# Performance work log

Hardware: AMD Instinct MI355X
Metric: run time of the kernel (lower is better)

The kernel has to match this reference:

```python
import jax, jax.numpy as jnp
import numpy as np

B, C, H, W = 4, 96, 64, 64
CS = 8                      # chunk size
DN = 2 * C                  # d_inner (expand=2)
N = 16                      # d_state
K = 4                       # scan directions
DT_R = (C + 15) // 16       # dt_rank = ceil(d_model/16)
EPS = 1e-5


def _ln(x, g, b):
    m = x.mean(-1, keepdims=True)
    v = ((x - m) ** 2).mean(-1, keepdims=True)
    return (x - m) / jnp.sqrt(v + EPS) * g + b


def _selective_scan(xs, delta, A, Bs, Cs, D):
    # xs, delta: (Bc, K, Dn, L); Bs, Cs: (Bc, K, N, L); A: (K, Dn, N); D: (K, Dn)
    Bc, Kk, Dn, L = xs.shape
    uT = xs.transpose(3, 0, 1, 2)       # (L, Bc, K, Dn)
    dT = delta.transpose(3, 0, 1, 2)
    BT = Bs.transpose(3, 0, 1, 2)       # (L, Bc, K, N)
    CT = Cs.transpose(3, 0, 1, 2)

    def step(h, inp):
        u_l, d_l, B_l, C_l = inp
        dA = jnp.exp(d_l[..., None] * A)                       # (Bc,K,Dn,N)
        h = h * dA + (d_l * u_l)[..., None] * B_l[:, :, None, :]
        y = jnp.einsum('bkdn,bkn->bkd', h, C_l)
        return h, y

    h0 = jnp.zeros((Bc, Kk, Dn, A.shape[-1]), xs.dtype)
    _, ys = jax.lax.scan(step, h0, (uT, dT, BT, CT))           # ys: (L,Bc,K,Dn)
    ys = ys.transpose(1, 2, 3, 0)                              # (Bc,K,Dn,L)
    return ys + D[None, :, :, None] * xs


def _ss2d(xh, in_proj_w, conv_w, conv_b, x_proj_w, dt_w, dt_b,
          A_logs, Ds, outnorm_g, outnorm_b, out_proj_w):
    # xh: (Bc, Hc, Wc, C)
    Bc, Hc, Wc, _ = xh.shape
    L = Hc * Wc
    xz = xh @ in_proj_w                                        # (Bc,Hc,Wc,2*Dn)
    xc, z = jnp.split(xz, 2, axis=-1)
    xc = xc.transpose(0, 3, 1, 2)                              # (Bc,Dn,Hc,Wc)
    xc = jax.lax.conv_general_dilated(xc, conv_w, (1, 1), ((1, 1), (1, 1)),
                                      feature_group_count=DN)
    xc = jax.nn.silu(xc + conv_b[None, :, None, None])
    x0 = xc.reshape(Bc, DN, L)                                 # HW order
    x1 = xc.transpose(0, 1, 3, 2).reshape(Bc, DN, L)           # WH order
    xs = jnp.stack([x0, x1, x0[:, :, ::-1], x1[:, :, ::-1]], axis=1)  # (Bc,4,Dn,L)
    x_dbl = jnp.einsum('bkdl,kcd->bkcl', xs, x_proj_w)         # (Bc,4,DT_R+2N,L)
    dts = x_dbl[:, :, :DT_R]
    Bs = x_dbl[:, :, DT_R:DT_R + N]
    Cs = x_dbl[:, :, DT_R + N:]
    dts = jnp.einsum('bkrl,kdr->bkdl', dts, dt_w)
    delta = jax.nn.softplus(dts + dt_b[None, :, :, None])      # (Bc,4,Dn,L)
    A = -jnp.exp(A_logs).reshape(K, DN, N)
    ys = _selective_scan(xs, delta, A, Bs, Cs, Ds.reshape(K, DN))
    y0 = ys[:, 0]
    y1 = ys[:, 1].reshape(Bc, DN, Wc, Hc).transpose(0, 1, 3, 2).reshape(Bc, DN, L)
    y2 = ys[:, 2, :, ::-1]
    y3 = ys[:, 3, :, ::-1].reshape(Bc, DN, Wc, Hc).transpose(0, 1, 3, 2).reshape(Bc, DN, L)
    y = (y0 + y1 + y2 + y3).transpose(0, 2, 1)                 # (Bc,L,Dn)
    y = _ln(y, outnorm_g, outnorm_b).reshape(Bc, Hc, Wc, DN)
    y = y * jax.nn.silu(z)
    return y @ out_proj_w                                      # (Bc,Hc,Wc,C)


def reference(x, gamma, beta, alpha, ln1_g, ln1_b, in_proj_w, conv_w, conv_b,
              x_proj_w, dt_w, dt_b, A_logs, Ds, outnorm_g, outnorm_b, out_proj_w):
    Bb, Cc, Hh, Ww = x.shape
    # StateNorm: per (b, c) over spatial dims, unbiased=False
    mean = x.mean(axis=(2, 3), keepdims=True)
    var = ((x - mean) ** 2).mean(axis=(2, 3), keepdims=True)
    x_norm = (x - mean) / jnp.sqrt(var + EPS)
    x_norm = gamma[None, :, None, None] * x_norm + beta[None, :, None, None]
    x_act = jax.nn.silu(x_norm)                 # act_quant with bits=32 is identity
    hn, wn = Hh // CS, Ww // CS
    # chunk: b c (hn cs)(wn cs) -> (b hn wn) c cs cs
    xc = x_act.reshape(Bb, Cc, hn, CS, wn, CS).transpose(0, 2, 4, 1, 3, 5)
    xc = xc.reshape(Bb * hn * wn, Cc, CS, CS)
    # VSSBlock: h + SS2D(LN(h)) in BHWC (drop_path = identity at inference)
    h = xc.transpose(0, 2, 3, 1)                # (Bc, cs, cs, C)
    h = h + _ss2d(_ln(h, ln1_g, ln1_b), in_proj_w, conv_w, conv_b, x_proj_w,
                  dt_w, dt_b, A_logs, Ds, outnorm_g, outnorm_b, out_proj_w)
    xv = h.transpose(0, 3, 1, 2)                # back to BCHW
    # unchunk
    xv = xv.reshape(Bb, hn, wn, Cc, CS, CS).transpose(0, 3, 1, 4, 2, 5)
    xv = xv.reshape(Bb, Cc, Hh, Ww)
    return x + alpha * xv


def setup_inputs() -> dict:
    key = jax.random.key(0)
    ks = jax.random.split(key, 12)
    s = 0.02
    inp = {
        'x': jax.random.normal(ks[0], (B, C, H, W), jnp.float32),
        'gamma': jnp.ones((C,), jnp.float32),
        'beta': jnp.zeros((C,), jnp.float32),
        'alpha': jnp.float32(0.5),
        'ln1_g': jnp.ones((C,), jnp.float32),
        'ln1_b': jnp.zeros((C,), jnp.float32),
        'in_proj_w': jax.random.normal(ks[1], (C, 2 * DN), jnp.float32) / np.sqrt(C),
        'conv_w': jax.random.normal(ks[2], (DN, 1, 3, 3), jnp.float32) / 3.0,
        'conv_b': jnp.zeros((DN,), jnp.float32),
        'x_proj_w': jax.random.normal(ks[3], (K, DT_R + 2 * N, DN), jnp.float32) / np.sqrt(DN),
        'dt_w': jax.random.normal(ks[4], (K, DN, DT_R), jnp.float32) * (DT_R ** -0.5),
        'dt_b': jnp.full((K, DN), -4.6, jnp.float32) + s * jax.random.normal(ks[5], (K, DN), jnp.float32),
        'A_logs': jnp.log(jnp.broadcast_to(jnp.arange(1, N + 1, dtype=jnp.float32), (K * DN, N))).copy(),
        'Ds': jnp.ones((K * DN,), jnp.float32),
        'outnorm_g': jnp.ones((DN,), jnp.float32),
        'outnorm_b': jnp.zeros((DN,), jnp.float32),
        'out_proj_w': jax.random.normal(ks[6], (DN, C), jnp.float32) / np.sqrt(DN),
    }
    return inp
```

## Files before the change

kernel.cpp:

```cpp
#include <hip/hip_runtime.h>
#include <math.h>

__device__ __forceinline__ float siluf_(float x) {
    return x / (1.f + __expf(-x));
}

__device__ __forceinline__ int sperm(int k, int l) {
    int t = (k & 1) ? (((l & 7) << 3) | (l >> 3)) : l;
    return (k & 2) ? (63 - t) : t;
}

__device__ __forceinline__ unsigned int f2bf(float f) {
    unsigned int u = __float_as_uint(f);
    return (u + 0x7FFFu + ((u >> 16) & 1u)) >> 16;
}
__device__ __forceinline__ float bf2f(unsigned int h) {
    return __uint_as_float(h << 16);
}
__device__ __forceinline__ unsigned int packbf(float lo, float hi) {
    return f2bf(lo) | (f2bf(hi) << 16);
}

__global__ void k1a_stats(const float* __restrict__ x, float* __restrict__ stats) {
    int bc = blockIdx.x;
    const float* xp = x + (size_t)bc * 4096;
    float s = 0.f, sq = 0.f;
    for (int i = threadIdx.x; i < 4096; i += 256) {
        float v = xp[i]; s += v; sq += v * v;
    }
    __shared__ float rs[256], rq[256];
    rs[threadIdx.x] = s; rq[threadIdx.x] = sq;
    __syncthreads();
    for (int off = 128; off > 0; off >>= 1) {
        if (threadIdx.x < off) {
            rs[threadIdx.x] += rs[threadIdx.x + off];
            rq[threadIdx.x] += rq[threadIdx.x + off];
        }
        __syncthreads();
    }
    if (threadIdx.x == 0) {
        float m = rs[0] * (1.f / 4096.f);
        float v = rq[0] * (1.f / 4096.f) - m * m;
        stats[bc] = m;
        stats[384 + bc] = rsqrtf(v + 1e-5f);
    }
}

__global__ __launch_bounds__(256) void kAB(
        const float* __restrict__ x, const float* __restrict__ stats,
        const float* __restrict__ gamma, const float* __restrict__ beta,
        const float* __restrict__ ln1_g, const float* __restrict__ ln1_b,
        const float* __restrict__ Win,
        const float* __restrict__ conv_w, const float* __restrict__ conv_b,
        float* __restrict__ x0T_all,
        unsigned int* __restrict__ zg_b) {
    int blk = blockIdx.x;
    int xcd = blk & 7, j = blk >> 3;
    int chunk = xcd * 32 + (j >> 1), cg = j & 1;
    int b = chunk >> 6, chh = (chunk >> 3) & 7, chw = chunk & 7;
    __shared__ float hs[64 * 97];
    __shared__ float xc[96 * 65];
    int t = threadIdx.x;
    for (int i = t; i < 6144; i += 256) {
        int c = i >> 6, pos = i & 63;
        int bc = b * 96 + c;
        int hh = chh * 8 + (pos >> 3), ww = chw * 8 + (pos & 7);
        float v = x[(((size_t)bc) * 64 + hh) * 64 + ww];
        float xn = (v - stats[bc]) * stats[384 + bc] * gamma[c] + beta[c];
        hs[pos * 97 + c] = siluf_(xn);
    }
    __syncthreads();
    {
        int p = t >> 2, o = t & 3;
        float s = 0.f, sq = 0.f;
        #pragma unroll
        for (int jj = 0; jj < 24; jj++) { float v = hs[p * 97 + o + 4 * jj]; s += v; sq += v * v; }
        s += __shfl_xor(s, 1); sq += __shfl_xor(sq, 1);
        s += __shfl_xor(s, 2); sq += __shfl_xor(sq, 2);
        float m = s * (1.f / 96.f);
        float rinv = rsqrtf(sq * (1.f / 96.f) - m * m + 1e-5f);
        #pragma unroll
        for (int jj = 0; jj < 24; jj++) {
            int c = o + 4 * jj;
            hs[p * 97 + c] = (hs[p * 97 + c] - m) * rinv * ln1_g[c] + ln1_b[c];
        }
    }
    __syncthreads();
    {
        int p = t & 63;
        int wv = __builtin_amdgcn_readfirstlane(t >> 6);
        int jc = cg * 96 + wv * 24;
        int jz = 192 + jc;
        float acc[48];
        #pragma unroll
        for (int i = 0; i < 48; i++) acc[i] = 0.f;
        for (int c = 0; c < 96; c++) {
            float u = hs[p * 97 + c];
            const float* w = Win + c * 384;
            #pragma unroll
            for (int i = 0; i < 24; i++) acc[i] = fmaf(u, w[jc + i], acc[i]);
            #pragma unroll
            for (int i = 0; i < 24; i++) acc[24 + i] = fmaf(u, w[jz + i], acc[24 + i]);
        }
        #pragma unroll
        for (int i = 0; i < 24; i++) xc[(wv * 24 + i) * 65 + p] = acc[i];
        int i2base = cg * 48 + wv * 12;
        unsigned int* o_ = zg_b + (size_t)chunk * 6144 + i2base * 64 + p;
        #pragma unroll
        for (int m2 = 0; m2 < 12; m2++)
            o_[m2 * 64] = packbf(acc[24 + 2 * m2], acc[24 + 2 * m2 + 1]);
    }
    __syncthreads();
    {
        float* x0o = x0T_all + (size_t)chunk * 12288 + cg * 96;
        for (int s = 0; s < 24; s++) {
            int idx = s * 256 + t;
            int l = idx / 96, dl = idx - l * 96;
            int d = cg * 96 + dl;
            int r = l >> 3, cc = l & 7;
            float acc = conv_b[d];
            #pragma unroll
            for (int dh = 0; dh < 3; dh++) {
                int rr = r + dh - 1;
                if (rr < 0 || rr > 7) continue;
                #pragma unroll
                for (int dw = 0; dw < 3; dw++) {
                    int cw = cc + dw - 1;
                    if (cw < 0 || cw > 7) continue;
                    acc = fmaf(xc[dl * 65 + rr * 8 + cw], conv_w[d * 9 + dh * 3 + dw], acc);
                }
            }
            x0o[l * 192 + dl] = siluf_(acc);
        }
    }
}

__global__ __launch_bounds__(384, 6) void kD(
        const float* __restrict__ x0T_all, const float* __restrict__ xpw,
        const float* __restrict__ dtw, const float* __restrict__ dtb,
        const float* __restrict__ A_logs, const float* __restrict__ Ds,
        unsigned int* __restrict__ yk01,
        unsigned int* __restrict__ yk23) {
    int blk = blockIdx.x;
    int xcd = blk & 7, j = blk >> 3;
    int chunk = xcd * 32 + (j >> 2);
    int k = j & 3;
    __shared__ float pT[64 * 40];
    int t = threadIdx.x;
    const float* xbase = x0T_all + (size_t)chunk * 12288;

    {
        int l = t & 63;
        int wv6 = __builtin_amdgcn_readfirstlane(t >> 6);
        int cbase = wv6 * 7;
        float acc[7];
        #pragma unroll
        for (int i = 0; i < 7; i++) acc[i] = 0.f;
        const float* xl = xbase + l * 192;
        const float* wb = xpw + (size_t)k * 38 * 192;
        for (int dd = 0; dd < 192; dd += 4) {
            float4 u4 = *(const float4*)(xl + dd);
            #pragma unroll
            for (int ci = 0; ci < 7; ci++) {
                int c = cbase + ci;
                if (c < 38) {
                    float4 w4 = *(const float4*)(wb + c * 192 + dd);
                    acc[ci] = fmaf(u4.x, w4.x, acc[ci]);
                    acc[ci] = fmaf(u4.y, w4.y, acc[ci]);
                    acc[ci] = fmaf(u4.z, w4.z, acc[ci]);
                    acc[ci] = fmaf(u4.w, w4.w, acc[ci]);
                }
            }
        }
        #pragma unroll
        for (int ci = 0; ci < 7; ci++) {
            int c = cbase + ci;
            if (c < 38) {
                int slot = c + (c >= 6 ? 2 : 0);
                pT[l * 40 + slot] = acc[ci];
            }
        }
    }
    __syncthreads();

    {
        int d = t >> 1, h = t & 1;
        int gd = k * 192 + d;
        float w6[6];
        #pragma unroll
        for (int r = 0; r < 6; r++) w6[r] = dtw[gd * 6 + r];
        float bias = dtb[gd];
        float Dd_eff = h ? 0.f : Ds[gd];
        float a0 = -__expf(A_logs[gd * 16]);
        float a8[8];
        #pragma unroll
        for (int n = 0; n < 8; n++) a8[n] = -__expf(A_logs[gd * 16 + 8 * h + n]);
        bool pw = true;
        #pragma unroll
        for (int n = 0; n < 8; n++) {
            float tgt = (float)(8 * h + n + 1) * a0;
            pw = pw && (fabsf(a8[n] - tgt) <= 1e-4f * fabsf(tgt) + 1e-6f);
        }
        bool a0m1 = (a0 == -1.0f);
        float c0 = a0 * (float)(8 * h + 1);
        float hst[8];
        #pragma unroll
        for (int n = 0; n < 8; n++) hst[n] = 0.f;
        unsigned int* yb = (k < 2 ? yk01 : yk23) + (size_t)(k & 1) * 1572864
                           + (size_t)chunk * 6144;
        int hb = 8 * h;

        if (__all(pw && a0m1)) {
            for (int g8 = 0; g8 < 8; ++g8) {
                float u8[8];
                #pragma unroll
                for (int i = 0; i < 8; i++)
                    u8[i] = xbase[sperm(k, g8 * 8 + i) * 192 + d];
                #pragma unroll
                for (int i = 0; i < 8; i += 2) {
                    int sl0 = sperm(k, g8 * 8 + i);
                    int sl1 = sperm(k, g8 * 8 + i + 1);
                    const float* row0 = pT + sl0 * 40;
                    const float* row1 = pT + sl1 * 40;
                    float4 rA0 = *(const float4*)(row0);
                    float2 rB0 = *(const float2*)(row0 + 4);
                    float4 b00 = *(const float4*)(row0 + 8 + hb);
                    float4 b01 = *(const float4*)(row0 + 12 + hb);
                    float4 c00 = *(const float4*)(row0 + 24 + hb);
                    float4 c01 = *(const float4*)(row0 + 28 + hb);
                    float4 rA1 = *(const float4*)(row1);
                    float2 rB1 = *(const float2*)(row1 + 4);
                    float4 b10 = *(const float4*)(row1 + 8 + hb);
                    float4 b11 = *(const float4*)(row1 + 12 + hb);
                    float4 c10 = *(const float4*)(row1 + 24 + hb);
                    float4 c11 = *(const float4*)(row1 + 28 + hb);
                    float dp0 = bias, dp1 = bias;
                    dp0 = fmaf(rA0.x, w6[0], dp0); dp1 = fmaf(rA1.x, w6[0], dp1);
                    dp0 = fmaf(rA0.y, w6[1], dp0); dp1 = fmaf(rA1.y, w6[1], dp1);
                    dp0 = fmaf(rA0.z, w6[2], dp0); dp1 = fmaf(rA1.z, w6[2], dp1);
                    dp0 = fmaf(rA0.w, w6[3], dp0); dp1 = fmaf(rA1.w, w6[3], dp1);
                    dp0 = fmaf(rB0.x, w6[4], dp0); dp1 = fmaf(rB1.x, w6[4], dp1);
                    dp0 = fmaf(rB0.y, w6[5], dp0); dp1 = fmaf(rB1.y, w6[5], dp1);
                    float ex0 = __expf(dp0), ex1 = __expf(dp1);
                    float delta0 = (dp0 > 20.f) ? dp0 : __logf(1.f + ex0);
                    float delta1 = (dp1 > 20.f) ? dp1 : __logf(1.f + ex1);
                    float e10 = __builtin_amdgcn_rcpf(1.f + ex0);
                    float e11 = __builtin_amdgcn_rcpf(1.f + ex1);
                    float du0 = delta0 * u8[i];
                    float du1 = delta1 * u8[i + 1];
                    float e20 = e10 * e10, e40 = e20 * e20, e80 = e40 * e40;
                    float ebm0 = e80 * e10;
                    float eb0 = h ? ebm0 : e10;
                    float p0 = eb0,       p1 = eb0 * e10, p2 = eb0 * e20, p3 = p1 * e20;
                    float p4 = eb0 * e40, p5 = p1 * e40,  p6 = p2 * e40,  p7 = p3 * e40;
                    float e21 = e11 * e11, e41 = e21 * e21, e81 = e41 * e41;
                    float ebm1 = e81 * e11;
                    float eb1 = h ? ebm1 : e11;
                    float q0 = eb1,       q1 = eb1 * e11, q2 = eb1 * e21, q3 = q1 * e21;
                    float q4 = eb1 * e41, q5 = q1 * e41,  q6 = q2 * e41,  q7 = q3 * e41;
                    float ya, yb_;
                    hst[0] = fmaf(hst[0], p0, du0 * b00.x); ya  = hst[0] * c00.x;
                    hst[1] = fmaf(hst[1], p1, du0 * b00.y); yb_ = hst[1] * c00.y;
                    hst[2] = fmaf(hst[2], p2, du0 * b00.z); ya  = fmaf(hst[2], c00.z, ya);
                    hst[3] = fmaf(hst[3], p3, du0 * b00.w); yb_ = fmaf(hst[3], c00.w, yb_);
                    hst[4] = fmaf(hst[4], p4, du0 * b01.x); ya  = fmaf(hst[4], c01.x, ya);
                    hst[5] = fmaf(hst[5], p5, du0 * b01.y); yb_ = fmaf(hst[5], c01.y, yb_);
                    hst[6] = fmaf(hst[6], p6, du0 * b01.z); ya  = fmaf(hst[6], c01.z, ya);
                    hst[7] = fmaf(hst[7], p7, du0 * b01.w); yb_ = fmaf(hst[7], c01.w, yb_);
                    float yp0 = fmaf(Dd_eff, u8[i], ya + yb_);
                    float yf0 = yp0 + __shfl_xor(yp0, 1);
                    float yo0 = __shfl_xor(yf0, 2);
                    if ((t & 3) == 0) yb[sl0 * 96 + (d >> 1)] = packbf(yf0, yo0);
                    hst[0] = fmaf(hst[0], q0, du1 * b10.x); ya  = hst[0] * c10.x;
                    hst[1] = fmaf(hst[1], q1, du1 * b10.y); yb_ = hst[1] * c10.y;
                    hst[2] = fmaf(hst[2], q2, du1 * b10.z); ya  = fmaf(hst[2], c10.z, ya);
                    hst[3] = fmaf(hst[3], q3, du1 * b10.w); yb_ = fmaf(hst[3], c10.w, yb_);
                    hst[4] = fmaf(hst[4], q4, du1 * b11.x); ya  = fmaf(hst[4], c11.x, ya);
                    hst[5] = fmaf(hst[5], q5, du1 * b11.y); yb_ = fmaf(hst[5], c11.y, yb_);
                    hst[6] = fmaf(hst[6], q6, du1 * b11.z); ya  = fmaf(hst[6], c11.z, ya);
                    hst[7] = fmaf(hst[7], q7, du1 * b11.w); yb_ = fmaf(hst[7], c11.w, yb_);
                    float yp1 = fmaf(Dd_eff, u8[i + 1], ya + yb_);
                    float yf1 = yp1 + __shfl_xor(yp1, 1);
                    float yo1 = __shfl_xor(yf1, 2);
                    if ((t & 3) == 0) yb[sl1 * 96 + (d >> 1)] = packbf(yf1, yo1);
                }
            }
        } else if (__all(pw)) {
            for (int g8 = 0; g8 < 8; ++g8) {
                float u8[8];
                #pragma unroll
                for (int i = 0; i < 8; i++)
                    u8[i] = xbase[sperm(k, g8 * 8 + i) * 192 + d];
                #pragma unroll
                for (int i = 0; i < 8; i++) {
                    int sl = sperm(k, g8 * 8 + i);
                    const float* row = pT + sl * 40;
                    float4 rA = *(const float4*)(row);
                    float2 rB = *(const float2*)(row + 4);
                    float dp = bias;
                    dp = fmaf(rA.x, w6[0], dp); dp = fmaf(rA.y, w6[1], dp);
                    dp = fmaf(rA.z, w6[2], dp); dp = fmaf(rA.w, w6[3], dp);
                    dp = fmaf(rB.x, w6[4], dp); dp = fmaf(rB.y, w6[5], dp);
                    float delta = (dp > 20.f) ? dp : __logf(1.f + __expf(dp));
                    float du = delta * u8[i];
                    float e1 = __expf(delta * a0);
                    float eb = __expf(delta * c0);
                    float e2 = e1 * e1, e4 = e2 * e2;
                    float p0 = eb,      p1 = eb * e1, p2 = eb * e2, p3 = p1 * e2;
                    float p4 = p0 * e4, p5 = p1 * e4, p6 = p2 * e4, p7 = p3 * e4;
                    float4 bq0 = *(const float4*)(row + 8 + hb);
                    float4 bq1 = *(const float4*)(row + 12 + hb);
                    float4 cq0 = *(const float4*)(row + 24 + hb);
                    float4 cq1 = *(const float4*)(row + 28 + hb);
                    float y0, y1;
                    hst[0] = fmaf(hst[0], p0, du * bq0.x); y0 = hst[0] * cq0.x;
                    hst[1] = fmaf(hst[1], p1, du * bq0.y); y1 = hst[1] * cq0.y;
                    hst[2] = fmaf(hst[2], p2, du * bq0.z); y0 = fmaf(hst[2], cq0.z, y0);
                    hst[3] = fmaf(hst[3], p3, du * bq0.w); y1 = fmaf(hst[3], cq0.w, y1);
                    hst[4] = fmaf(hst[4], p4, du * bq1.x); y0 = fmaf(hst[4], cq1.x, y0);
                    hst[5] = fmaf(hst[5], p5, du * bq1.y); y1 = fmaf(hst[5], cq1.y, y1);
                    hst[6] = fmaf(hst[6], p6, du * bq1.z); y0 = fmaf(hst[6], cq1.z, y0);
                    hst[7] = fmaf(hst[7], p7, du * bq1.w); y1 = fmaf(hst[7], cq1.w, y1);
                    float yp = fmaf(Dd_eff, u8[i], y0 + y1);
                    float yfull = yp + __shfl_xor(yp, 1);
                    float yo2 = __shfl_xor(yfull, 2);
                    if ((t & 3) == 0) yb[sl * 96 + (d >> 1)] = packbf(yfull, yo2);
                }
            }
        } else {
            for (int l = 0; l < 64; l++) {
                int sl = sperm(k, l);
                float u = xbase[sl * 192 + d];
                const float* row = pT + sl * 40;
                float dp = bias;
                #pragma unroll
                for (int r = 0; r < 6; r++) dp = fmaf(row[r], w6[r], dp);
                float delta = (dp > 20.f) ? dp : __logf(1.f + __expf(dp));
                float du = delta * u;
                float yp = 0.f;
                #pragma unroll
                for (int n = 0; n < 8; n++) {
                    float e = __expf(delta * a8[n]);
                    hst[n] = fmaf(hst[n], e, du * row[8 + hb + n]);
                    yp = fmaf(hst[n], row[24 + hb + n], yp);
                }
                yp = fmaf(Dd_eff, u, yp);
                float yfull = yp + __shfl_xor(yp, 1);
                float yo2 = __shfl_xor(yfull, 2);
                if ((t & 3) == 0) yb[sl * 96 + (d >> 1)] = packbf(yfull, yo2);
            }
        }
    }
}

__global__ __launch_bounds__(256) void kEF(
        const unsigned int* __restrict__ yk01, const unsigned int* __restrict__ yk23,
        const unsigned int* __restrict__ zg_b,
        const float* __restrict__ og, const float* __restrict__ ob,
        const float* __restrict__ Wout,
        const float* __restrict__ x, const float* __restrict__ stats,
        const float* __restrict__ gamma, const float* __restrict__ beta,
        const float* __restrict__ alpha, float* __restrict__ out) {
    int blk = blockIdx.x;
    int xcd = blk & 7, j = blk >> 3;
    int chunk = xcd * 32 + (j >> 1), cgf = j & 1;
    int b = chunk >> 6, chh = (chunk >> 3) & 7, chw = chunk & 7;
    __shared__ float gs[64 * 193];
    int t = threadIdx.x;
    for (int half = 0; half < 2; half++) {
        int p = half * 32 + (t >> 3), o = t & 7;
        int par = o & 1;
        size_t rb = (size_t)chunk * 6144 + p * 96;
        const unsigned int* r0 = yk01 + rb;
        const unsigned int* r1 = yk01 + 1572864 + rb;
        const unsigned int* r2 = yk23 + rb;
        const unsigned int* r3 = yk23 + 1572864 + rb;
        float ys[24];
        float s = 0.f, sq = 0.f;
        #pragma unroll
        for (int jj = 0; jj < 24; jj++) {
            int i = o + 8 * jj;
            int wi = i >> 1;
            int sh = par ? 16 : 0;
            float v = bf2f((r0[wi] >> sh) & 0xFFFFu) + bf2f((r1[wi] >> sh) & 0xFFFFu)
                    + bf2f((r2[wi] >> sh) & 0xFFFFu) + bf2f((r3[wi] >> sh) & 0xFFFFu);
            ys[jj] = v; s += v; sq += v * v;
        }
        s += __shfl_xor(s, 1); sq += __shfl_xor(sq, 1);
        s += __shfl_xor(s, 2); sq += __shfl_xor(sq, 2);
        s += __shfl_xor(s, 4); sq += __shfl_xor(sq, 4);
        float m = s * (1.f / 192.f);
        float rinv = rsqrtf(sq * (1.f / 192.f) - m * m + 1e-5f);
        const unsigned int* z = zg_b + (size_t)chunk * 6144;
        #pragma unroll
        for (int jj = 0; jj < 24; jj++) {
            int i = o + 8 * jj;
            float ln = (ys[jj] - m) * rinv * og[i] + ob[i];
            unsigned int zw = z[(i >> 1) * 64 + p];
            float zv = bf2f(par ? (zw >> 16) : (zw & 0xFFFFu));
            gs[p * 193 + i] = ln * siluf_(zv);
        }
    }
    __syncthreads();
    {
        int p = t & 63;
        int wv = __builtin_amdgcn_readfirstlane(t >> 6);
        int cbase = cgf * 48 + wv * 12;
        float acc[12];
        #pragma unroll
        for (int i = 0; i < 12; i++) acc[i] = 0.f;
        for (int dd = 0; dd < 192; dd++) {
            float u = gs[p * 193 + dd];
            const float* w = Wout + dd * 96 + cbase;
            #pragma unroll
            for (int i = 0; i < 12; i++) acc[i] = fmaf(u, w[i], acc[i]);
        }
        float al = alpha[0];
        int hh = chh * 8 + (p >> 3), ww = chw * 8 + (p & 7);
        #pragma unroll
        for (int i = 0; i < 12; i++) {
            int c = cbase + i;
            int bc = b * 96 + c;
            size_t gi = (((size_t)bc) * 64 + hh) * 64 + ww;
            float xv = x[gi];
            float xn = (xv - stats[bc]) * stats[384 + bc] * gamma[c] + beta[c];
            out[gi] = xv + al * (siluf_(xn) + acc[i]);
        }
    }
}

extern "C" void kernel_launch(void* const* d_in, const int* in_sizes, int n_in,
                              void* d_out, int out_size, void* d_ws, size_t ws_size,
                              hipStream_t stream) {
    const float* x        = (const float*)d_in[0];
    const float* gamma    = (const float*)d_in[1];
    const float* beta     = (const float*)d_in[2];
    const float* alpha    = (const float*)d_in[3];
    const float* ln1_g    = (const float*)d_in[4];
    const float* ln1_b    = (const float*)d_in[5];
    const float* in_proj  = (const float*)d_in[6];
    const float* conv_w   = (const float*)d_in[7];
    const float* conv_b   = (const float*)d_in[8];
    const float* x_proj   = (const float*)d_in[9];
    const float* dt_w     = (const float*)d_in[10];
    const float* dt_b     = (const float*)d_in[11];
    const float* A_logs   = (const float*)d_in[12];
    const float* Ds       = (const float*)d_in[13];
    const float* onorm_g  = (const float*)d_in[14];
    const float* onorm_b  = (const float*)d_in[15];
    const float* out_proj = (const float*)d_in[16];
    float* out = (float*)d_out;

    float* ws    = (float*)d_ws;
    float* stats = ws;
    float* x0T   = ws + 768;
    unsigned int* zg_b = (unsigned int*)(x0T + 3145728);
    unsigned int* yk01 = zg_b + 1572864;
    unsigned int* yk23 = yk01 + 3145728;

    hipLaunchKernelGGL(k1a_stats, dim3(384), dim3(256), 0, stream, x, stats);
    hipLaunchKernelGGL(kAB, dim3(512), dim3(256), 0, stream,
                       x, stats, gamma, beta, ln1_g, ln1_b, in_proj,
                       conv_w, conv_b, x0T, zg_b);
    hipLaunchKernelGGL(kD, dim3(1024), dim3(384), 0, stream,
                       x0T, x_proj, dt_w, dt_b, A_logs, Ds, yk01, yk23);
    hipLaunchKernelGGL(kEF, dim3(512), dim3(256), 0, stream,
                       yk01, yk23, zg_b, onorm_g, onorm_b, out_proj,
                       x, stats, gamma, beta, alpha, out);
}
```

Measured before the change: 202.3 us.

## Split kAB and kEF work over more blocks, pack scan B/C to bf16

kAB now splits each chunk's projection channels into four quarter-blocks instead of two, and kEF splits both pixels and output channels so each chunk is covered by four blocks. Both launch 1024 blocks with fewer accumulators per thread. The aim is more parallelism and occupancy, paid for by recomputing the LayerNorm prologue in each extra block. In kD, the projected B and C values are repacked into bf16 pairs in a second shared array, which halves the LDS reads per scan step but adds a repack pass, a barrier and bf16 rounding of B and C.

```diff
diff --git a/kernel.cpp b/kernel.cpp
--- a/kernel.cpp
+++ b/kernel.cpp
@@ -20,6 +20,8 @@
 __device__ __forceinline__ unsigned int packbf(float lo, float hi) {
     return f2bf(lo) | (f2bf(hi) << 16);
 }
+__device__ __forceinline__ float bflo(unsigned int u) { return __uint_as_float(u << 16); }
+__device__ __forceinline__ float bfhi(unsigned int u) { return __uint_as_float(u & 0xFFFF0000u); }
 
 __global__ void k1a_stats(const float* __restrict__ x, float* __restrict__ stats) {
     int bc = blockIdx.x;
@@ -56,10 +58,10 @@
         unsigned int* __restrict__ zg_b) {
     int blk = blockIdx.x;
     int xcd = blk & 7, j = blk >> 3;
-    int chunk = xcd * 32 + (j >> 1), cg = j & 1;
+    int chunk = xcd * 32 + (j >> 2), q = j & 3;
     int b = chunk >> 6, chh = (chunk >> 3) & 7, chw = chunk & 7;
     __shared__ float hs[64 * 97];
-    __shared__ float xc[96 * 65];
+    __shared__ float xc[48 * 65];
     int t = threadIdx.x;
     for (int i = t; i < 6144; i += 256) {
         int c = i >> 6, pos = i & 63;
@@ -89,34 +91,34 @@
     {
         int p = t & 63;
         int wv = __builtin_amdgcn_readfirstlane(t >> 6);
-        int jc = cg * 96 + wv * 24;
+        int jc = q * 48 + wv * 12;
         int jz = 192 + jc;
-        float acc[48];
-        #pragma unroll
-        for (int i = 0; i < 48; i++) acc[i] = 0.f;
+        float acc[24];
+        #pragma unroll
+        for (int i = 0; i < 24; i++) acc[i] = 0.f;
         for (int c = 0; c < 96; c++) {
             float u = hs[p * 97 + c];
             const float* w = Win + c * 384;
             #pragma unroll
-            for (int i = 0; i < 24; i++) acc[i] = fmaf(u, w[jc + i], acc[i]);
+            for (int i = 0; i < 12; i++) acc[i] = fmaf(u, w[jc + i], acc[i]);
             #pragma unroll
-            for (int i = 0; i < 24; i++) acc[24 + i] = fmaf(u, w[jz + i], acc[24 + i]);
-        }
-        #pragma unroll
-        for (int i = 0; i < 24; i++) xc[(wv * 24 + i) * 65 + p] = acc[i];
-        int i2base = cg * 48 + wv * 12;
+            for (int i = 0; i < 12; i++) acc[12 + i] = fmaf(u, w[jz + i], acc[12 + i]);
+        }
+        #pragma unroll
+        for (int i = 0; i < 12; i++) xc[(wv * 12 + i) * 65 + p] = acc[i];
+        int i2base = q * 24 + wv * 6;
         unsigned int* o_ = zg_b + (size_t)chunk * 6144 + i2base * 64 + p;
         #pragma unroll
-        for (int m2 = 0; m2 < 12; m2++)
-            o_[m2 * 64] = packbf(acc[24 + 2 * m2], acc[24 + 2 * m2 + 1]);
-    }
-    __syncthreads();
-    {
-        float* x0o = x0T_all + (size_t)chunk * 12288 + cg * 96;
-        for (int s = 0; s < 24; s++) {
+        for (int m2 = 0; m2 < 6; m2++)
+            o_[m2 * 64] = packbf(acc[12 + 2 * m2], acc[12 + 2 * m2 + 1]);
+    }
+    __syncthreads();
+    {
+        float* x0o = x0T_all + (size_t)chunk * 12288 + q * 48;
+        for (int s = 0; s < 12; s++) {
             int idx = s * 256 + t;
-            int l = idx / 96, dl = idx - l * 96;
-            int d = cg * 96 + dl;
+            int l = idx / 48, dl = idx - l * 48;
+            int d = q * 48 + dl;
             int r = l >> 3, cc = l & 7;
             float acc = conv_b[d];
             #pragma unroll
@@ -146,6 +148,7 @@
     int chunk = xcd * 32 + (j >> 2);
     int k = j & 3;
     __shared__ float pT[64 * 40];
+    __shared__ unsigned int pTp[64 * 24];
     int t = threadIdx.x;
     const float* xbase = x0T_all + (size_t)chunk * 12288;
 
@@ -182,6 +185,23 @@
         }
     }
     __syncthreads();
+    for (int i = t; i < 1536; i += 384) {
+        int l = i / 24, s = i - l * 24;
+        unsigned int v = 0;
+        if (s < 6) v = __float_as_uint(pT[l * 40 + s]);
+        else if (s >= 8) {
+            int qq = s - 8;
+            int half = qq >> 3;
+            int w = qq & 7;
+            int isC = w >> 2;
+            int pr = w & 3;
+            int n = half * 8 + pr * 2;
+            int slot = (isC ? 24 : 8) + n;
+            v = packbf(pT[l * 40 + slot], pT[l * 40 + slot + 1]);
+        }
+        pTp[i] = v;
+    }
+    __syncthreads();
 
     {
         int d = t >> 1, h = t & 1;
@@ -220,20 +240,16 @@
                 for (int i = 0; i < 8; i += 2) {
                     int sl0 = sperm(k, g8 * 8 + i);
                     int sl1 = sperm(k, g8 * 8 + i + 1);
-                    const float* row0 = pT + sl0 * 40;
-                    const float* row1 = pT + sl1 * 40;
+                    const unsigned int* row0 = pTp + sl0 * 24;
+                    const unsigned int* row1 = pTp + sl1 * 24;
                     float4 rA0 = *(const float4*)(row0);
-                    float2 rB0 = *(const float2*)(row0 + 4);
-                    float4 b00 = *(const float4*)(row0 + 8 + hb);
-                    float4 b01 = *(const float4*)(row0 + 12 + hb);
-                    float4 c00 = *(const float4*)(row0 + 24 + hb);
-                    float4 c01 = *(const float4*)(row0 + 28 + hb);
+                    float2 rB0 = *(const float2*)((const float*)row0 + 4);
+                    uint4 Bp0 = *(const uint4*)(row0 + 8 + h * 8);
+                    uint4 Cp0 = *(const uint4*)(row0 + 12 + h * 8);
                     float4 rA1 = *(const float4*)(row1);
-                    float2 rB1 = *(const float2*)(row1 + 4);
-                    float4 b10 = *(const float4*)(row1 + 8 + hb);
-                    float4 b11 = *(const float4*)(row1 + 12 + hb);
-                    float4 c10 = *(const float4*)(row1 + 24 + hb);
-                    float4 c11 = *(const float4*)(row1 + 28 + hb);
+                    float2 rB1 = *(const float2*)((const float*)row1 + 4);
+                    uint4 Bp1 = *(const uint4*)(row1 + 8 + h * 8);
+                    uint4 Cp1 = *(const uint4*)(row1 + 12 + h * 8);
                     float dp0 = bias, dp1 = bias;
                     dp0 = fmaf(rA0.x, w6[0], dp0); dp1 = fmaf(rA1.x, w6[0], dp1);
                     dp0 = fmaf(rA0.y, w6[1], dp0); dp1 = fmaf(rA1.y, w6[1], dp1);
@@ -248,37 +264,35 @@
                     float e11 = __builtin_amdgcn_rcpf(1.f + ex1);
                     float du0 = delta0 * u8[i];
                     float du1 = delta1 * u8[i + 1];
-                    float e20 = e10 * e10, e40 = e20 * e20, e80 = e40 * e40;
-                    float ebm0 = e80 * e10;
-                    float eb0 = h ? ebm0 : e10;
+                    float e20 = e10 * e10, e40 = e20 * e20;
+                    float eb0 = h ? (e40 * e40 * e10) : e10;
                     float p0 = eb0,       p1 = eb0 * e10, p2 = eb0 * e20, p3 = p1 * e20;
                     float p4 = eb0 * e40, p5 = p1 * e40,  p6 = p2 * e40,  p7 = p3 * e40;
-                    float e21 = e11 * e11, e41 = e21 * e21, e81 = e41 * e41;
-                    float ebm1 = e81 * e11;
-                    float eb1 = h ? ebm1 : e11;
+                    float e21 = e11 * e11, e41 = e21 * e21;
+                    float eb1 = h ? (e41 * e41 * e11) : e11;
                     float q0 = eb1,       q1 = eb1 * e11, q2 = eb1 * e21, q3 = q1 * e21;
                     float q4 = eb1 * e41, q5 = q1 * e41,  q6 = q2 * e41,  q7 = q3 * e41;
                     float ya, yb_;
-                    hst[0] = fmaf(hst[0], p0, du0 * b00.x); ya  = hst[0] * c00.x;
-                    hst[1] = fmaf(hst[1], p1, du0 * b00.y); yb_ = hst[1] * c00.y;
-                    hst[2] = fmaf(hst[2], p2, du0 * b00.z); ya  = fmaf(hst[2], c00.z, ya);
-                    hst[3] = fmaf(hst[3], p3, du0 * b00.w); yb_ = fmaf(hst[3], c00.w, yb_);
-                    hst[4] = fmaf(hst[4], p4, du0 * b01.x); ya  = fmaf(hst[4], c01.x, ya);
-                    hst[5] = fmaf(hst[5], p5, du0 * b01.y); yb_ = fmaf(hst[5], c01.y, yb_);
-                    hst[6] = fmaf(hst[6], p6, du0 * b01.z); ya  = fmaf(hst[6], c01.z, ya);
-                    hst[7] = fmaf(hst[7], p7, du0 * b01.w); yb_ = fmaf(hst[7], c01.w, yb_);
+                    hst[0] = fmaf(hst[0], p0, du0 * bflo(Bp0.x)); ya  = hst[0] * bflo(Cp0.x);
+                    hst[1] = fmaf(hst[1], p1, du0 * bfhi(Bp0.x)); yb_ = hst[1] * bfhi(Cp0.x);
+                    hst[2] = fmaf(hst[2], p2, du0 * bflo(Bp0.y)); ya  = fmaf(hst[2], bflo(Cp0.y), ya);
+                    hst[3] = fmaf(hst[3], p3, du0 * bfhi(Bp0.y)); yb_ = fmaf(hst[3], bfhi(Cp0.y), yb_);
+                    hst[4] = fmaf(hst[4], p4, du0 * bflo(Bp0.z)); ya  = fmaf(hst[4], bflo(Cp0.z), ya);
+                    hst[5] = fmaf(hst[5], p5, du0 * bfhi(Bp0.z)); yb_ = fmaf(hst[5], bfhi(Cp0.z), yb_);
+                    hst[6] = fmaf(hst[6], p6, du0 * bflo(Bp0.w)); ya  = fmaf(hst[6], bflo(Cp0.w), ya);
+                    hst[7] = fmaf(hst[7], p7, du0 * bfhi(Bp0.w)); yb_ = fmaf(hst[7], bfhi(Cp0.w), yb_);
                     float yp0 = fmaf(Dd_eff, u8[i], ya + yb_);
                     float yf0 = yp0 + __shfl_xor(yp0, 1);
                     float yo0 = __shfl_xor(yf0, 2);
                     if ((t & 3) == 0) yb[sl0 * 96 + (d >> 1)] = packbf(yf0, yo0);
-                    hst[0] = fmaf(hst[0], q0, du1 * b10.x); ya  = hst[0] * c10.x;
-                    hst[1] = fmaf(hst[1], q1, du1 * b10.y); yb_ = hst[1] * c10.y;
-                    hst[2] = fmaf(hst[2], q2, du1 * b10.z); ya  = fmaf(hst[2], c10.z, ya);
-                    hst[3] = fmaf(hst[3], q3, du1 * b10.w); yb_ = fmaf(hst[3], c10.w, yb_);
-                    hst[4] = fmaf(hst[4], q4, du1 * b11.x); ya  = fmaf(hst[4], c11.x, ya);
-                    hst[5] = fmaf(hst[5], q5, du1 * b11.y); yb_ = fmaf(hst[5], c11.y, yb_);
-                    hst[6] = fmaf(hst[6], q6, du1 * b11.z); ya  = fmaf(hst[6], c11.z, ya);
-                    hst[7] = fmaf(hst[7], q7, du1 * b11.w); yb_ = fmaf(hst[7], c11.w, yb_);
+                    hst[0] = fmaf(hst[0], q0, du1 * bflo(Bp1.x)); ya  = hst[0] * bflo(Cp1.x);
+                    hst[1] = fmaf(hst[1], q1, du1 * bfhi(Bp1.x)); yb_ = hst[1] * bfhi(Cp1.x);
+                    hst[2] = fmaf(hst[2], q2, du1 * bflo(Bp1.y)); ya  = fmaf(hst[2], bflo(Cp1.y), ya);
+                    hst[3] = fmaf(hst[3], q3, du1 * bfhi(Bp1.y)); yb_ = fmaf(hst[3], bfhi(Cp1.y), yb_);
+                    hst[4] = fmaf(hst[4], q4, du1 * bflo(Bp1.z)); ya  = fmaf(hst[4], bflo(Cp1.z), ya);
+                    hst[5] = fmaf(hst[5], q5, du1 * bfhi(Bp1.z)); yb_ = fmaf(hst[5], bfhi(Cp1.z), yb_);
+                    hst[6] = fmaf(hst[6], q6, du1 * bflo(Bp1.w)); ya  = fmaf(hst[6], bflo(Cp1.w), ya);
+                    hst[7] = fmaf(hst[7], q7, du1 * bfhi(Bp1.w)); yb_ = fmaf(hst[7], bfhi(Cp1.w), yb_);
                     float yp1 = fmaf(Dd_eff, u8[i + 1], ya + yb_);
                     float yf1 = yp1 + __shfl_xor(yp1, 1);
                     float yo1 = __shfl_xor(yf1, 2);
@@ -363,12 +377,14 @@
         const float* __restrict__ alpha, float* __restrict__ out) {
     int blk = blockIdx.x;
     int xcd = blk & 7, j = blk >> 3;
-    int chunk = xcd * 32 + (j >> 1), cgf = j & 1;
+    int chunk = xcd * 32 + (j >> 2);
+    int ph = (j >> 1) & 1, ch = j & 1;
     int b = chunk >> 6, chh = (chunk >> 3) & 7, chw = chunk & 7;
-    __shared__ float gs[64 * 193];
+    __shared__ float gs[32 * 193];
     int t = threadIdx.x;
-    for (int half = 0; half < 2; half++) {
-        int p = half * 32 + (t >> 3), o = t & 7;
+    {
+        int pl = t >> 3, o = t & 7;
+        int p = ph * 32 + pl;
         int par = o & 1;
         size_t rb = (size_t)chunk * 6144 + p * 96;
         const unsigned int* r0 = yk01 + rb;
@@ -398,27 +414,28 @@
             float ln = (ys[jj] - m) * rinv * og[i] + ob[i];
             unsigned int zw = z[(i >> 1) * 64 + p];
             float zv = bf2f(par ? (zw >> 16) : (zw & 0xFFFFu));
-            gs[p * 193 + i] = ln * siluf_(zv);
-        }
-    }
-    __syncthreads();
-    {
-        int p = t & 63;
-        int wv = __builtin_amdgcn_readfirstlane(t >> 6);
-        int cbase = cgf * 48 + wv * 12;
-        float acc[12];
-        #pragma unroll
-        for (int i = 0; i < 12; i++) acc[i] = 0.f;
+            gs[pl * 193 + i] = ln * siluf_(zv);
+        }
+    }
+    __syncthreads();
+    {
+        int pl = t & 31;
+        int g32 = t >> 5;
+        int cbase = ch * 48 + g32 * 6;
+        float acc[6];
+        #pragma unroll
+        for (int i = 0; i < 6; i++) acc[i] = 0.f;
         for (int dd = 0; dd < 192; dd++) {
-            float u = gs[p * 193 + dd];
+            float u = gs[pl * 193 + dd];
             const float* w = Wout + dd * 96 + cbase;
             #pragma unroll
-            for (int i = 0; i < 12; i++) acc[i] = fmaf(u, w[i], acc[i]);
+            for (int i = 0; i < 6; i++) acc[i] = fmaf(u, w[i], acc[i]);
         }
         float al = alpha[0];
+        int p = ph * 32 + pl;
         int hh = chh * 8 + (p >> 3), ww = chw * 8 + (p & 7);
         #pragma unroll
-        for (int i = 0; i < 12; i++) {
+        for (int i = 0; i < 6; i++) {
             int c = cbase + i;
             int bc = b * 96 + c;
             size_t gi = (((size_t)bc) * 64 + hh) * 64 + ww;
@@ -459,12 +476,12 @@
     unsigned int* yk23 = yk01 + 3145728;
 
     hipLaunchKernelGGL(k1a_stats, dim3(384), dim3(256), 0, stream, x, stats);
-    hipLaunchKernelGGL(kAB, dim3(512), dim3(256), 0, stream,
+    hipLaunchKernelGGL(kAB, dim3(1024), dim3(256), 0, stream,
                        x, stats, gamma, beta, ln1_g, ln1_b, in_proj,
                        conv_w, conv_b, x0T, zg_b);
     hipLaunchKernelGGL(kD, dim3(1024), dim3(384), 0, stream,
                        x0T, x_proj, dt_w, dt_b, A_logs, Ds, yk01, yk23);
-    hipLaunchKernelGGL(kEF, dim3(512), dim3(256), 0, stream,
+    hipLaunchKernelGGL(kEF, dim3(1024), dim3(256), 0, stream,
                        yk01, yk23, zg_b, onorm_g, onorm_b, out_proj,
                        x, stats, gamma, beta, alpha, out);
 }
```

Result: slower. 233.1 us (+15.2%).
